# Performance work log

Hardware: AMD Instinct MI355X
Metric: run time of the kernel (lower is better)

Reference implementation:

```python
import jax, jax.numpy as jnp
import numpy as np

N, C_IN, C_OUT, K = 8192, 128, 128, 3


def setup_inputs() -> dict:
    key = jax.random.key(0)
    k1, k2, k3 = jax.random.split(key, 3)
    x = jax.random.normal(k1, (N, C_IN), dtype=jnp.float32)
    # scale L by 1/sqrt(N) so the Chebyshev recurrence stays numerically tame
    L = jax.random.normal(k2, (N, N), dtype=jnp.float32) / np.sqrt(N).astype(np.float32)
    # stacked per-order linear weights, W[j] has shape [out, in] like nn.Linear.weight
    W = jax.random.normal(k3, (K, C_OUT, C_IN), dtype=jnp.float32) / np.sqrt(C_IN).astype(np.float32)
    return {"x": x, "L": L, "W": W}


def reference(x, L, W):
    # Chebyshev polynomial recurrence: T_0 = x, T_1 = L x, T_j = 2 L T_{j-1} - T_{j-2}
    # out = sum_j T_j @ W[j].T
    k = W.shape[0]  # static
    T0 = x
    T1 = L @ x
    out = T0 @ W[0].T
    if k > 1:
        out = out + T1 @ W[1].T
    for j in range(2, k):
        T2 = 2.0 * (L @ T1) - T0
        out = out + T2 @ W[j].T
        T0, T1 = T1, T2
    return out
```

## Files before the change

kernel.cpp:

```cpp
#include <hip/hip_runtime.h>

typedef __attribute__((ext_vector_type(8))) short short8;
typedef __attribute__((ext_vector_type(4))) float float4_t;
typedef __attribute__((ext_vector_type(4))) unsigned short ushort4_t;

#define NR 8192
#define C 128
#define SPLITK 8
#define KCHUNK (NR / SPLITK)
#define BK 64

__device__ unsigned short g_xbT[(size_t)C * NR];
__device__ unsigned short g_T1b[(size_t)NR * C];
__device__ unsigned short g_T1bT[(size_t)C * NR];
__device__ unsigned short g_Wb[3 * C * C];
__device__ unsigned short g_Lb[(size_t)NR * NR];
__device__ float g_part[(size_t)SPLITK * NR * C];

__device__ __forceinline__ unsigned short f2bf(float f) {
  union { float f; unsigned u; } v; v.f = f;
  unsigned r = v.u + 0x7fffu + ((v.u >> 16) & 1u);
  return (unsigned short)(r >> 16);
}
__device__ __forceinline__ unsigned pk2(float a, float b) {
  union { float f; unsigned u; } x, y; x.f = a; y.f = b;
  unsigned ra = x.u + 0x7fffu + ((x.u >> 16) & 1u);
  unsigned rb = y.u + 0x7fffu + ((y.u >> 16) & 1u);
  return (ra >> 16) | (rb & 0xffff0000u);
}
__device__ __forceinline__ short8 cvt8(float4_t f0, float4_t f1) {
  union { unsigned u[4]; short8 s; } r;
  r.u[0] = pk2(f0[0], f0[1]); r.u[1] = pk2(f0[2], f0[3]);
  r.u[2] = pk2(f1[0], f1[1]); r.u[3] = pk2(f1[2], f1[3]);
  return r.s;
}

typedef __attribute__((address_space(3))) unsigned lds_uint;
typedef const __attribute__((address_space(1))) unsigned glob_uint;
__device__ __forceinline__ void gload_lds16(const void* g, void* l) {
  __builtin_amdgcn_global_load_lds((glob_uint*)g, (lds_uint*)l, 16, 0, 0);
}

__global__ void cvt_w(const float* __restrict__ W) {
  int i = (blockIdx.x * 256 + threadIdx.x) * 4;
  float4_t v = *(const float4_t*)(W + i);
  ushort4_t h; h[0]=f2bf(v[0]); h[1]=f2bf(v[1]); h[2]=f2bf(v[2]); h[3]=f2bf(v[3]);
  *(ushort4_t*)(g_Wb + i) = h;
}

__global__ __launch_bounds__(256) void cvt_L(const float* __restrict__ L) {
  size_t i = ((size_t)blockIdx.x * 256 + threadIdx.x) * 8;
  float4_t f0 = *(const float4_t*)(L + i);
  float4_t f1 = *(const float4_t*)(L + i + 4);
  *(short8*)(g_Lb + i) = cvt8(f0, f1);
}

__global__ void transpose_x(const float* __restrict__ x) {
  __shared__ unsigned short xt[64][72];
  int r0 = blockIdx.x * 64;
  int c0 = blockIdx.y * 64;
  int t = threadIdx.x;
  int rr = t >> 4;
  int cc = (t & 15) * 4;
#pragma unroll
  for (int i = 0; i < 4; i++) {
    int row = i * 16 + rr;
    float4_t v = *(const float4_t*)(x + (size_t)(r0 + row) * C + c0 + cc);
    ushort4_t h; h[0]=f2bf(v[0]); h[1]=f2bf(v[1]); h[2]=f2bf(v[2]); h[3]=f2bf(v[3]);
    *(ushort4_t*)(&xt[row][cc]) = h;
  }
  __syncthreads();
  int c = t >> 2;
  int q = t & 3;
  unsigned short* dst = g_xbT + (size_t)(c0 + c) * NR + r0 + q * 16;
#pragma unroll
  for (int seg = 0; seg < 4; seg++) {
    ushort4_t h;
#pragma unroll
    for (int j = 0; j < 4; j++) h[j] = xt[q * 16 + seg * 4 + j][c];
    *(ushort4_t*)(dst + seg * 4) = h;
  }
}

__global__ __launch_bounds__(256, 4) void gemm_bf16(int which) {
  const unsigned short* __restrict__ BT = which ? g_T1bT : g_xbT;
  __shared__ __attribute__((aligned(16))) unsigned short As[64 * BK];
  __shared__ __attribute__((aligned(16))) unsigned short Bs[128 * BK];
  int tid = threadIdx.x;
  int wave = tid >> 6, lane = tid & 63;
  int l15 = lane & 15, lq = lane >> 4;
  int m0 = blockIdx.x * 64;
  int kb = blockIdx.y * KCHUNK;

  const unsigned short* pA[2];
#pragma unroll
  for (int i = 0; i < 2; i++) {
    int U = (wave * 2 + i) * 64 + lane;
    int row = U >> 3, p = U & 7;
    pA[i] = g_Lb + (size_t)(m0 + row) * NR + kb + ((p ^ (row & 7)) << 3);
  }
  const unsigned short* pB[4];
#pragma unroll
  for (int i = 0; i < 4; i++) {
    int U = (wave * 4 + i) * 64 + lane;
    int n = U >> 3, p = U & 7;
    pB[i] = BT + (size_t)n * NR + kb + ((p ^ (n & 7)) << 3);
  }

  float4_t acc[8];
#pragma unroll
  for (int ni = 0; ni < 8; ni++) acc[ni] = (float4_t){0.f, 0.f, 0.f, 0.f};

  for (int step = 0; step < KCHUNK / BK; step++) {
#pragma unroll
    for (int i = 0; i < 2; i++)
      gload_lds16(pA[i], (char*)As + (wave * 2 + i) * 1024);
#pragma unroll
    for (int i = 0; i < 4; i++)
      gload_lds16(pB[i], (char*)Bs + (wave * 4 + i) * 1024);
    __syncthreads();
#pragma unroll
    for (int ki = 0; ki < 2; ki++) {
      int row = wave * 16 + l15;
      int pa = ((ki << 2) | lq) ^ (row & 7);
      short8 a = *(const short8*)(As + row * 64 + pa * 8);
#pragma unroll
      for (int ni = 0; ni < 8; ni++) {
        int n = ni * 16 + l15;
        int pb = ((ki << 2) | lq) ^ (n & 7);
        short8 b = *(const short8*)(Bs + n * 64 + pb * 8);
        acc[ni] = __builtin_amdgcn_mfma_f32_16x16x32_bf16(a, b, acc[ni], 0, 0, 0);
      }
    }
    __syncthreads();
#pragma unroll
    for (int i = 0; i < 2; i++) pA[i] += BK;
#pragma unroll
    for (int i = 0; i < 4; i++) pB[i] += BK;
  }

  float* po = g_part + (size_t)blockIdx.y * NR * C;
#pragma unroll
  for (int ni = 0; ni < 8; ni++)
#pragma unroll
    for (int r = 0; r < 4; r++)
      po[(size_t)(m0 + wave * 16 + lq * 4 + r) * C + ni * 16 + l15] = acc[ni][r];
}

__global__ void reduce_t1() {
  __shared__ unsigned short tile[16][132];
  int r0 = blockIdx.x * 16;
  int t = threadIdx.x;
#pragma unroll
  for (int e = 0; e < 2; e++) {
    int linear = e * 1024 + t * 4;
    int r = linear >> 7, c = linear & 127;
    float4_t s = (float4_t){0.f, 0.f, 0.f, 0.f};
#pragma unroll
    for (int p = 0; p < SPLITK; p++)
      s += *(const float4_t*)(g_part + (size_t)p * NR * C + (size_t)(r0 + r) * C + c);
    ushort4_t h; h[0]=f2bf(s[0]); h[1]=f2bf(s[1]); h[2]=f2bf(s[2]); h[3]=f2bf(s[3]);
    *(ushort4_t*)(g_T1b + (size_t)(r0 + r) * C + c) = h;
    *(ushort4_t*)(&tile[r][c]) = h;
  }
  __syncthreads();
  int c = t >> 1, half = t & 1;
  unsigned short* dst = g_T1bT + (size_t)c * NR + r0 + half * 8;
#pragma unroll
  for (int seg = 0; seg < 2; seg++) {
    ushort4_t h;
#pragma unroll
    for (int j = 0; j < 4; j++) h[j] = tile[half * 8 + seg * 4 + j][c];
    *(ushort4_t*)(dst + seg * 4) = h;
  }
}

__global__ __launch_bounds__(256) void epilogue(const float* __restrict__ x,
                                                float* __restrict__ out) {
  __shared__ unsigned short t2[32][136];
  int r0 = blockIdx.x * 32;
  int t = threadIdx.x;
#pragma unroll
  for (int e = 0; e < 4; e++) {
    int linear = e * 1024 + t * 4;
    int r = linear >> 7, c = linear & 127;
    float4_t s = (float4_t){0.f, 0.f, 0.f, 0.f};
#pragma unroll
    for (int p = 0; p < SPLITK; p++)
      s += *(const float4_t*)(g_part + (size_t)p * NR * C + (size_t)(r0 + r) * C + c);
    float4_t xv = *(const float4_t*)(x + (size_t)(r0 + r) * C + c);
    float4_t t2v = 2.0f * s - xv;
    ushort4_t h; h[0]=f2bf(t2v[0]); h[1]=f2bf(t2v[1]); h[2]=f2bf(t2v[2]); h[3]=f2bf(t2v[3]);
    *(ushort4_t*)(&t2[r][c]) = h;
  }
  __syncthreads();

  int wave = t >> 6, lane = t & 63, l15 = lane & 15, lq = lane >> 4;
  int mf = wave & 1, nh = wave >> 1;
  int m0r = r0 + mf * 16;
  float4_t acc[4];
#pragma unroll
  for (int ni = 0; ni < 4; ni++) acc[ni] = (float4_t){0.f, 0.f, 0.f, 0.f};

#pragma unroll
  for (int ks = 0; ks < 4; ks++) {
    int k0 = ks * 32 + lq * 8;
    const float* px = x + (size_t)(m0r + l15) * C + k0;
    float4_t f0 = *(const float4_t*)px;
    float4_t f1 = *(const float4_t*)(px + 4);
    short8 a0 = cvt8(f0, f1);
    short8 a1 = *(const short8*)(g_T1b + (size_t)(m0r + l15) * C + k0);
    short8 a2 = *(const short8*)(&t2[mf * 16 + l15][k0]);
#pragma unroll
    for (int ni = 0; ni < 4; ni++) {
      int n = nh * 64 + ni * 16 + l15;
      const unsigned short* pw = g_Wb + (size_t)n * C + k0;
      short8 w0 = *(const short8*)(pw);
      short8 w1 = *(const short8*)(pw + C * C);
      short8 w2 = *(const short8*)(pw + 2 * C * C);
      acc[ni] = __builtin_amdgcn_mfma_f32_16x16x32_bf16(a0, w0, acc[ni], 0, 0, 0);
      acc[ni] = __builtin_amdgcn_mfma_f32_16x16x32_bf16(a1, w1, acc[ni], 0, 0, 0);
      acc[ni] = __builtin_amdgcn_mfma_f32_16x16x32_bf16(a2, w2, acc[ni], 0, 0, 0);
    }
  }
#pragma unroll
  for (int ni = 0; ni < 4; ni++)
#pragma unroll
    for (int r = 0; r < 4; r++)
      out[(size_t)(m0r + lq * 4 + r) * C + nh * 64 + ni * 16 + l15] = acc[ni][r];
}

extern "C" void kernel_launch(void* const* d_in, const int* in_sizes, int n_in,
                              void* d_out, int out_size, void* d_ws, size_t ws_size,
                              hipStream_t stream) {
  const float* x = (const float*)d_in[0];
  const float* L = (const float*)d_in[1];
  const float* W = (const float*)d_in[2];
  float* out = (float*)d_out;

  cvt_w<<<48, 256, 0, stream>>>(W);
  transpose_x<<<dim3(128, 2), 256, 0, stream>>>(x);
  cvt_L<<<32768, 256, 0, stream>>>(L);
  gemm_bf16<<<dim3(128, SPLITK), 256, 0, stream>>>(0);
  reduce_t1<<<512, 256, 0, stream>>>();
  gemm_bf16<<<dim3(128, SPLITK), 256, 0, stream>>>(1);
  epilogue<<<256, 256, 0, stream>>>(x, out);
}
```

Before: 509.5 us.

## Fuse L bf16 conversion into GEMM loads and double-buffer LDS staging

Drops the separate pass that converts L to bf16. Each GEMM now streams fp32 L into LDS and converts it in registers before the MFMA. The main loop gains double-buffered asynchronous global-to-LDS loads with explicit waitcnt and barriers, so loads overlap compute. Split-K falls from 8 to 4, which halves the partial traffic at the cost of fewer blocks and more LDS per block.

```diff
diff --git a/kernel.cpp b/kernel.cpp
--- a/kernel.cpp
+++ b/kernel.cpp
@@ -6,15 +6,15 @@
 
 #define NR 8192
 #define C 128
-#define SPLITK 8
+#define SPLITK 4
 #define KCHUNK (NR / SPLITK)
 #define BK 64
+#define STEPS (KCHUNK / BK)
 
 __device__ unsigned short g_xbT[(size_t)C * NR];
 __device__ unsigned short g_T1b[(size_t)NR * C];
 __device__ unsigned short g_T1bT[(size_t)C * NR];
 __device__ unsigned short g_Wb[3 * C * C];
-__device__ unsigned short g_Lb[(size_t)NR * NR];
 __device__ float g_part[(size_t)SPLITK * NR * C];
 
 __device__ __forceinline__ unsigned short f2bf(float f) {
@@ -46,13 +46,6 @@
   float4_t v = *(const float4_t*)(W + i);
   ushort4_t h; h[0]=f2bf(v[0]); h[1]=f2bf(v[1]); h[2]=f2bf(v[2]); h[3]=f2bf(v[3]);
   *(ushort4_t*)(g_Wb + i) = h;
-}
-
-__global__ __launch_bounds__(256) void cvt_L(const float* __restrict__ L) {
-  size_t i = ((size_t)blockIdx.x * 256 + threadIdx.x) * 8;
-  float4_t f0 = *(const float4_t*)(L + i);
-  float4_t f1 = *(const float4_t*)(L + i + 4);
-  *(short8*)(g_Lb + i) = cvt8(f0, f1);
 }
 
 __global__ void transpose_x(const float* __restrict__ x) {
@@ -70,34 +63,33 @@
     *(ushort4_t*)(&xt[row][cc]) = h;
   }
   __syncthreads();
-  int c = t >> 2;
-  int q = t & 3;
+  int c = t >> 2, q = t & 3;
   unsigned short* dst = g_xbT + (size_t)(c0 + c) * NR + r0 + q * 16;
 #pragma unroll
-  for (int seg = 0; seg < 4; seg++) {
-    ushort4_t h;
-#pragma unroll
-    for (int j = 0; j < 4; j++) h[j] = xt[q * 16 + seg * 4 + j][c];
-    *(ushort4_t*)(dst + seg * 4) = h;
-  }
-}
-
-__global__ __launch_bounds__(256, 4) void gemm_bf16(int which) {
+  for (int seg = 0; seg < 2; seg++) {
+    short8 h;
+#pragma unroll
+    for (int j = 0; j < 8; j++) h[j] = (short)xt[q * 16 + seg * 8 + j][c];
+    *(short8*)(dst + seg * 8) = h;
+  }
+}
+
+__global__ __launch_bounds__(256, 2) void gemm_cheb(const float* __restrict__ L, int which) {
   const unsigned short* __restrict__ BT = which ? g_T1bT : g_xbT;
-  __shared__ __attribute__((aligned(16))) unsigned short As[64 * BK];
-  __shared__ __attribute__((aligned(16))) unsigned short Bs[128 * BK];
+  __shared__ __attribute__((aligned(16))) float          As[2][64 * BK];
+  __shared__ __attribute__((aligned(16))) unsigned short Bs[2][128 * BK];
   int tid = threadIdx.x;
   int wave = tid >> 6, lane = tid & 63;
   int l15 = lane & 15, lq = lane >> 4;
   int m0 = blockIdx.x * 64;
   int kb = blockIdx.y * KCHUNK;
 
-  const unsigned short* pA[2];
-#pragma unroll
-  for (int i = 0; i < 2; i++) {
-    int U = (wave * 2 + i) * 64 + lane;
-    int row = U >> 3, p = U & 7;
-    pA[i] = g_Lb + (size_t)(m0 + row) * NR + kb + ((p ^ (row & 7)) << 3);
+  const float* pA[4];
+#pragma unroll
+  for (int i = 0; i < 4; i++) {
+    int U = (wave * 4 + i) * 64 + lane;
+    int row = U >> 4, p = U & 15;
+    pA[i] = L + (size_t)(m0 + row) * NR + kb + ((p ^ (row & 15)) << 2);
   }
   const unsigned short* pB[4];
 #pragma unroll
@@ -111,33 +103,50 @@
 #pragma unroll
   for (int ni = 0; ni < 8; ni++) acc[ni] = (float4_t){0.f, 0.f, 0.f, 0.f};
 
-  for (int step = 0; step < KCHUNK / BK; step++) {
-#pragma unroll
-    for (int i = 0; i < 2; i++)
-      gload_lds16(pA[i], (char*)As + (wave * 2 + i) * 1024);
-#pragma unroll
-    for (int i = 0; i < 4; i++)
-      gload_lds16(pB[i], (char*)Bs + (wave * 4 + i) * 1024);
-    __syncthreads();
-#pragma unroll
-    for (int ki = 0; ki < 2; ki++) {
-      int row = wave * 16 + l15;
-      int pa = ((ki << 2) | lq) ^ (row & 7);
-      short8 a = *(const short8*)(As + row * 64 + pa * 8);
-#pragma unroll
-      for (int ni = 0; ni < 8; ni++) {
-        int n = ni * 16 + l15;
-        int pb = ((ki << 2) | lq) ^ (n & 7);
-        short8 b = *(const short8*)(Bs + n * 64 + pb * 8);
-        acc[ni] = __builtin_amdgcn_mfma_f32_16x16x32_bf16(a, b, acc[ni], 0, 0, 0);
-      }
-    }
-    __syncthreads();
-#pragma unroll
-    for (int i = 0; i < 2; i++) pA[i] += BK;
-#pragma unroll
-    for (int i = 0; i < 4; i++) pB[i] += BK;
-  }
+  #define ISSUE(buf)                                                         \
+    do {                                                                     \
+      _Pragma("unroll")                                                      \
+      for (int i = 0; i < 4; i++)                                            \
+        gload_lds16(pA[i], (char*)&As[buf][0] + (wave * 4 + i) * 1024);      \
+      _Pragma("unroll")                                                      \
+      for (int i = 0; i < 4; i++)                                            \
+        gload_lds16(pB[i], (char*)&Bs[buf][0] + (wave * 4 + i) * 1024);      \
+      _Pragma("unroll")                                                      \
+      for (int i = 0; i < 4; i++) { pA[i] += BK; pB[i] += BK; }              \
+    } while (0)
+
+  #define COMPUTE(buf)                                                       \
+    do {                                                                     \
+      _Pragma("unroll")                                                      \
+      for (int ki = 0; ki < 2; ki++) {                                       \
+        int row = wave * 16 + l15;                                           \
+        int u0 = (ki << 3) | (lq << 1);                                      \
+        int p0 = u0 ^ (row & 15);                                            \
+        float4_t f0 = *(const float4_t*)((const char*)&As[buf][0] + row * 256 + p0 * 16);        \
+        float4_t f1 = *(const float4_t*)((const char*)&As[buf][0] + row * 256 + (p0 ^ 1) * 16);  \
+        short8 a = cvt8(f0, f1);                                             \
+        _Pragma("unroll")                                                    \
+        for (int ni = 0; ni < 8; ni++) {                                     \
+          int n = ni * 16 + l15;                                             \
+          int pb = ((ki << 2) | lq) ^ (n & 7);                               \
+          short8 b = *(const short8*)((const char*)&Bs[buf][0] + n * 128 + pb * 16);             \
+          acc[ni] = __builtin_amdgcn_mfma_f32_16x16x32_bf16(a, b, acc[ni], 0, 0, 0);             \
+        }                                                                    \
+      }                                                                      \
+    } while (0)
+
+  ISSUE(0);
+  for (int step = 0; step < STEPS - 1; step++) {
+    int p = step & 1;
+    ISSUE(p ^ 1);
+    asm volatile("s_waitcnt vmcnt(8)" ::: "memory");
+    asm volatile("s_barrier" ::: "memory");
+    COMPUTE(p);
+    asm volatile("s_barrier" ::: "memory");
+  }
+  asm volatile("s_waitcnt vmcnt(0)" ::: "memory");
+  asm volatile("s_barrier" ::: "memory");
+  COMPUTE((STEPS - 1) & 1);
 
   float* po = g_part + (size_t)blockIdx.y * NR * C;
 #pragma unroll
@@ -145,10 +154,12 @@
 #pragma unroll
     for (int r = 0; r < 4; r++)
       po[(size_t)(m0 + wave * 16 + lq * 4 + r) * C + ni * 16 + l15] = acc[ni][r];
+  #undef ISSUE
+  #undef COMPUTE
 }
 
 __global__ void reduce_t1() {
-  __shared__ unsigned short tile[16][132];
+  __shared__ unsigned short tile[16][136];
   int r0 = blockIdx.x * 16;
   int t = threadIdx.x;
 #pragma unroll
@@ -165,14 +176,10 @@
   }
   __syncthreads();
   int c = t >> 1, half = t & 1;
-  unsigned short* dst = g_T1bT + (size_t)c * NR + r0 + half * 8;
-#pragma unroll
-  for (int seg = 0; seg < 2; seg++) {
-    ushort4_t h;
-#pragma unroll
-    for (int j = 0; j < 4; j++) h[j] = tile[half * 8 + seg * 4 + j][c];
-    *(ushort4_t*)(dst + seg * 4) = h;
-  }
+  short8 h;
+#pragma unroll
+  for (int j = 0; j < 8; j++) h[j] = (short)tile[half * 8 + j][c];
+  *(short8*)(g_T1bT + (size_t)c * NR + r0 + half * 8) = h;
 }
 
 __global__ __launch_bounds__(256) void epilogue(const float* __restrict__ x,
@@ -240,9 +247,8 @@
 
   cvt_w<<<48, 256, 0, stream>>>(W);
   transpose_x<<<dim3(128, 2), 256, 0, stream>>>(x);
-  cvt_L<<<32768, 256, 0, stream>>>(L);
-  gemm_bf16<<<dim3(128, SPLITK), 256, 0, stream>>>(0);
+  gemm_cheb<<<dim3(128, SPLITK), 256, 0, stream>>>(L, 0);
   reduce_t1<<<512, 256, 0, stream>>>();
-  gemm_bf16<<<dim3(128, SPLITK), 256, 0, stream>>>(1);
+  gemm_cheb<<<dim3(128, SPLITK), 256, 0, stream>>>(L, 1);
   epilogue<<<256, 256, 0, stream>>>(x, out);
 }
```

Measured after the change: 508.0 us. About the same (-0.3%).
